# Kernel tuning notes

Measured on AMD Instinct MI355X. Metric: run time of the kernel, lower is better.

## Reference

```python
import jax, jax.numpy as jnp
import numpy as np

# Constants matching init_kwargs: s=4 -> tuple_length t=1, k=2001
K = 2001          # encoded sequence length
T = 1             # tuple length (s=4)
B_SEQ = 2048      # number of sequences b (B = b*K)
M = 16            # models per row (last dim of inputs)
N = int(np.int32(1 + (K - T - 1) / 2))   # = 1000
OV = K - 2 * N                            # overlap length = 1
NUM_SEG = 6 * B_SEQ


def _build_seg_ids():
    # Per-sequence id pattern: n left frames cycling [0,1,2], overlap -> -1,
    # n right frames cycling [3,4,5]; sequence i gets offset 6*i (only on valid ids).
    left = np.resize(np.array([0, 1, 2], np.int32), N)
    right = np.resize(np.array([3, 4, 5], np.int32), N)
    per = np.concatenate([left, -np.ones(OV, np.int32), right])  # [K]
    offs = 6 * np.arange(B_SEQ, dtype=np.int32)[:, None]          # [b,1]
    ids = np.where(per[None, :] >= 0, per[None, :] + offs, -1)    # [b,K]
    return jnp.asarray(ids.reshape(-1))                            # [b*K]

SEG_IDS = _build_seg_ids()


def setup_inputs() -> dict:
    key = jax.random.key(0)
    inputs = jax.random.normal(key, (B_SEQ * K, M), dtype=jnp.float32)
    return {"inputs": inputs}


def reference(inputs) -> jnp.ndarray:
    valid = SEG_IDS >= 0                       # overlap rows dropped (like TF negative ids)
    safe_ids = jnp.where(valid, SEG_IDS, 0)
    w = valid.astype(inputs.dtype)             # [B]
    sums = jax.ops.segment_sum(inputs * w[:, None], safe_ids, num_segments=NUM_SEG)
    cnts = jax.ops.segment_sum(w, safe_ids, num_segments=NUM_SEG)
    mean = sums / jnp.maximum(cnts, 1.0)[:, None]   # unsorted_segment_mean (0 if empty)
    mean = jnp.where(cnts[:, None] > 0, mean, 0.0)
    return mean.reshape(B_SEQ, 6 * M)
```

## Files before the change

kernel.cpp:

```cpp
#include <hip/hip_runtime.h>


constexpr int K = 2001;
constexpr int M = 16;
constexpr int NSEQ = 2048;

typedef float v4f __attribute__((ext_vector_type(4)));

__global__ __launch_bounds__(384) void
seg_mean_kernel(const float* __restrict__ in, float* __restrict__ out) {
    const int b    = blockIdx.x;
    const int t    = threadIdx.x;
    const int g    = t >> 6;
    const int lane = t & 63;
    const int quad = lane & 3;
    const int ridx = lane >> 2;

    const int jbase = (g < 3) ? g : (998 + g);
    const int cnt   = (g == 0 || g == 3) ? 334 : 333;

    const v4f* __restrict__ base =
        reinterpret_cast<const v4f*>(in + (size_t)b * K * M);

    v4f acc = (v4f)(0.0f);
    for (int r = ridx; r < cnt; r += 16) {
        const int j = jbase + 3 * r;
        v4f v = __builtin_nontemporal_load(&base[j * 4 + quad]);
        acc += v;
    }

#pragma unroll
    for (int mask = 4; mask < 64; mask <<= 1) {
        acc[0] += __shfl_xor(acc[0], mask, 64);
        acc[1] += __shfl_xor(acc[1], mask, 64);
        acc[2] += __shfl_xor(acc[2], mask, 64);
        acc[3] += __shfl_xor(acc[3], mask, 64);
    }

    if (lane < 4) {
        const float inv = 1.0f / (float)cnt;
        v4f r4 = acc * inv;
        v4f* outv = reinterpret_cast<v4f*>(out + (size_t)b * 96 + g * 16);
        __builtin_nontemporal_store(r4, &outv[quad]);
    }
}

extern "C" void kernel_launch(void* const* d_in, const int* in_sizes, int n_in,
                              void* d_out, int out_size, void* d_ws, size_t ws_size,
                              hipStream_t stream) {
    const float* in = (const float*)d_in[0];
    float* out = (float*)d_out;
    seg_mean_kernel<<<NSEQ, 384, 0, stream>>>(in, out);
}
```

Before: 330.7 us.

## Stream sequence rows contiguously and reduce per-segment partials through LDS

Each block now has its threads read the sequence's float4 elements in a contiguous strided sweep rather than giving each wavefront a stride-3 row pattern. Because 384 is a multiple of 12, each thread always touches the same segment and column quad, so it keeps left and right accumulators. The partials are then combined through an LDS table and reduced by 24 threads. This aims at fully coalesced memory access, at the cost of a shared-memory reduction and a barrier.

New measurement: 322.7 us. 1.02x faster.

```diff
diff --git a/kernel.cpp b/kernel.cpp
--- a/kernel.cpp
+++ b/kernel.cpp
@@ -1,47 +1,60 @@
 #include <hip/hip_runtime.h>
 
 
-constexpr int K = 2001;
-constexpr int M = 16;
+constexpr int K    = 2001;
+constexpr int M    = 16;
 constexpr int NSEQ = 2048;
+constexpr int NV   = K * 4;
+constexpr int NT   = 384;
 
 typedef float v4f __attribute__((ext_vector_type(4)));
 
-__global__ __launch_bounds__(384) void
+__global__ __launch_bounds__(NT) void
 seg_mean_kernel(const float* __restrict__ in, float* __restrict__ out) {
-    const int b    = blockIdx.x;
-    const int t    = threadIdx.x;
-    const int g    = t >> 6;
-    const int lane = t & 63;
-    const int quad = lane & 3;
-    const int ridx = lane >> 2;
-
-    const int jbase = (g < 3) ? g : (998 + g);
-    const int cnt   = (g == 0 || g == 3) ? 334 : 333;
+    const int b = blockIdx.x;
+    const int t = threadIdx.x;
 
     const v4f* __restrict__ base =
         reinterpret_cast<const v4f*>(in + (size_t)b * K * M);
 
-    v4f acc = (v4f)(0.0f);
-    for (int r = ridx; r < cnt; r += 16) {
-        const int j = jbase + 3 * r;
-        v4f v = __builtin_nontemporal_load(&base[j * 4 + quad]);
-        acc += v;
+    v4f accL = (v4f)(0.0f);
+    v4f accR = (v4f)(0.0f);
+
+    for (int i = t; i < NV; i += NT) {
+        v4f v = __builtin_nontemporal_load(&base[i]);
+        const int j = i >> 2;
+        if (j < 1000) {
+            accL += v;
+        } else if (j > 1000) {
+            accR += v;
+        }
     }
 
+    __shared__ v4f lds[2][12][33];
+    const int key = t % 12;
+    const int m   = t / 12;
+    lds[0][key][m] = accL;
+    lds[1][key][m] = accR;
+    __syncthreads();
+
+    if (t < 24) {
+        const int region = t / 12;
+        const int k2     = t % 12;
+        const int c      = k2 >> 2;
+        const int q      = k2 & 3;
+
+        v4f s = (v4f)(0.0f);
 #pragma unroll
-    for (int mask = 4; mask < 64; mask <<= 1) {
-        acc[0] += __shfl_xor(acc[0], mask, 64);
-        acc[1] += __shfl_xor(acc[1], mask, 64);
-        acc[2] += __shfl_xor(acc[2], mask, 64);
-        acc[3] += __shfl_xor(acc[3], mask, 64);
-    }
+        for (int mm = 0; mm < 32; ++mm) {
+            s += lds[region][k2][(mm + k2) & 31];
+        }
 
-    if (lane < 4) {
-        const float inv = 1.0f / (float)cnt;
-        v4f r4 = acc * inv;
-        v4f* outv = reinterpret_cast<v4f*>(out + (size_t)b * 96 + g * 16);
-        __builtin_nontemporal_store(r4, &outv[quad]);
+        const int g = (region == 0) ? c : 3 + ((c + 1) % 3);
+        const float cnt = (g == 0 || g == 3) ? 334.0f : 333.0f;
+        v4f r = s * (1.0f / cnt);
+
+        v4f* o = reinterpret_cast<v4f*>(out + (size_t)b * 96 + g * 16 + q * 4);
+        __builtin_nontemporal_store(r, o);
     }
 }
 
@@ -50,5 +63,5 @@
                               hipStream_t stream) {
     const float* in = (const float*)d_in[0];
     float* out = (float*)d_out;
-    seg_mean_kernel<<<NSEQ, 384, 0, stream>>>(in, out);
+    seg_mean_kernel<<<NSEQ, NT, 0, stream>>>(in, out);
 }
```
